# Performance work log

Measured on AMD Instinct MI355X. Metric: run time of the kernel, lower is better.

Reference implementation:

```python
import jax, jax.numpy as jnp
import numpy as np

D_MODEL = 512
NHEAD = 8
HEAD_DIM = D_MODEL // NHEAD
DFF = 2048
RANK = 64
L = 1024
N = 8
EPS = 1e-5


def _layer_norm(x, g, b):
    m = jnp.mean(x, axis=-1, keepdims=True)
    v = jnp.mean(jnp.square(x - m), axis=-1, keepdims=True)
    return (x - m) * jax.lax.rsqrt(v + EPS) * g + b


def setup_inputs() -> dict:
    key = jax.random.key(0)
    ks = jax.random.split(key, 20)
    s = 1.0 / np.sqrt(D_MODEL)
    inp = {
        "q": jax.random.normal(ks[0], (L, N, D_MODEL), jnp.float32),
        "k": jax.random.normal(ks[1], (L, N, D_MODEL), jnp.float32),
        "v": jax.random.normal(ks[2], (L, N, D_MODEL), jnp.float32),
        # attention projections, stored (in, out) so x @ W
        "Wq": jax.random.normal(ks[3], (D_MODEL, D_MODEL), jnp.float32) * s,
        "bq": jnp.zeros((D_MODEL,), jnp.float32),
        "Wk": jax.random.normal(ks[4], (D_MODEL, D_MODEL), jnp.float32) * s,
        "bk": jnp.zeros((D_MODEL,), jnp.float32),
        "Wv": jax.random.normal(ks[5], (D_MODEL, D_MODEL), jnp.float32) * s,
        "bv": jnp.zeros((D_MODEL,), jnp.float32),
        "Wo": jax.random.normal(ks[6], (D_MODEL, D_MODEL), jnp.float32) * s,
        "bo": jnp.zeros((D_MODEL,), jnp.float32),
        "topk": jnp.float32(0.3),  # learned scalar, k = int(S * sigmoid(topk))
        "A1": jax.random.normal(ks[7], (D_MODEL, RANK), jnp.float32) * s,
        "B1": jax.random.normal(ks[8], (RANK, DFF), jnp.float32) / np.sqrt(RANK),
        "A2": jax.random.normal(ks[9], (DFF, RANK), jnp.float32) / np.sqrt(DFF),
        "B2": jax.random.normal(ks[10], (RANK, D_MODEL), jnp.float32) / np.sqrt(RANK),
        "g1": jnp.ones((D_MODEL,), jnp.float32),
        "be1": jnp.zeros((D_MODEL,), jnp.float32),
        "g2": jnp.ones((D_MODEL,), jnp.float32),
        "be2": jnp.zeros((D_MODEL,), jnp.float32),
    }
    return inp


def reference(q, k, v, Wq, bq, Wk, bk, Wv, bv, Wo, bo, topk,
              A1, B1, A2, B2, g1, be1, g2, be2):
    Lq, Nb, E = q.shape
    S = k.shape[0]
    H, Dh = NHEAD, HEAD_DIM

    # projections -> (N, L, H, Dh)
    qh = (q @ Wq + bq).reshape(Lq, Nb, H, Dh).transpose(1, 0, 2, 3)
    kh = (k @ Wk + bk).reshape(S, Nb, H, Dh).transpose(1, 0, 2, 3)
    vh = (v @ Wv + bv).reshape(S, Nb, H, Dh).transpose(1, 0, 2, 3)

    scores = jnp.einsum('nlhd,nshd->nlhs', qh, kh) / jnp.sqrt(jnp.float32(Dh))

    # dynamic top-k mask: keep the k = int(S * sigmoid(topk)) largest per row
    k_keep = (S * jax.nn.sigmoid(topk)).astype(jnp.int32)  # 588 for topk=0.3
    sorted_desc = jnp.sort(scores, axis=-1)[..., ::-1]
    idx = jnp.broadcast_to(k_keep - 1, scores.shape[:-1])[..., None]
    thresh = jnp.take_along_axis(sorted_desc, idx, axis=-1)  # k-th largest
    masked = jnp.where(scores >= thresh, scores, -jnp.inf)
    attn_w = jax.nn.softmax(masked, axis=-1)

    # note original flattens (d, h) order: 'nlhs,nshd->nldh' then view(L,N,E)
    ao = jnp.einsum('nlhs,nshd->nldh', attn_w, vh)
    ao = ao.transpose(1, 0, 2, 3).reshape(Lq, Nb, E)
    attn_out = ao @ Wo + bo

    src = _layer_norm(q + attn_out, g1, be1)
    ffn = jax.nn.relu(src @ A1 @ B1) @ A2 @ B2
    src = _layer_norm(src + ffn, g2, be2)
    return src
```

## Files before the change

### kernel.cpp

```cpp
#include <hip/hip_runtime.h>

typedef unsigned short u16;
typedef unsigned int u32;
typedef unsigned long long u64;
using s16x8 = __attribute__((ext_vector_type(8))) short;
using s16x4 = __attribute__((ext_vector_type(4))) short;
using u16x4 = __attribute__((ext_vector_type(4))) unsigned short;
using u32x4 = __attribute__((ext_vector_type(4))) unsigned int;
using f32x4 = __attribute__((ext_vector_type(4))) float;

__device__ __forceinline__ u16 f2bf(float f) {
  unsigned int u = __float_as_uint(f);
  u += 0x7FFFu + ((u >> 16) & 1u);
  return (u16)(u >> 16);
}
__device__ __forceinline__ float bf2f(u16 b) {
  return __uint_as_float(((u32)b) << 16);
}
__device__ __forceinline__ u32 pkbf(float a, float b) {
  u32 r;
  asm("v_cvt_pk_bf16_f32 %0, %1, %2" : "=v"(r) : "v"(a), "v"(b));
  return r;
}
__device__ __forceinline__ u64 cmp_ge(u32 key, u32 cand) {
  u64 m;
  asm("v_cmp_le_u32 %0, %1, %2" : "=s"(m) : "s"(cand), "v"(key));
  return m;
}
__device__ __forceinline__ u32 f2key(float f) {
  u32 u = __float_as_uint(f);
  u32 flip = (u32)((int)u >> 31) | 0x80000000u;
  return (u ^ flip) >> 16;
}
__device__ __forceinline__ float key2f(u32 k) {
  u32 t = k << 16;
  u32 msk = ((int)t < 0) ? 0x80000000u : 0xFFFF0000u;
  return __uint_as_float(t ^ msk);
}

__global__ __launch_bounds__(256) void prep_w(
    const float* __restrict__ Wq, const float* __restrict__ Wk, const float* __restrict__ Wv,
    const float* __restrict__ Wo, const float* __restrict__ A1, const float* __restrict__ B1,
    const float* __restrict__ A2, const float* __restrict__ B2,
    u16* __restrict__ WqT, u16* __restrict__ WkT, u16* __restrict__ WvT, u16* __restrict__ WoT,
    u16* __restrict__ A1T, u16* __restrict__ B1T, u16* __restrict__ A2T, u16* __restrict__ B2T) {
  __shared__ u16 t[64][68];
  int b = blockIdx.x, tid = threadIdx.x;
  const float* src; u16* dst; int base, R, C;
  if (b < 64)        { src = Wq; dst = WqT; base = 0;   R = 512;  C = 512; }
  else if (b < 128)  { src = Wk; dst = WkT; base = 64;  R = 512;  C = 512; }
  else if (b < 192)  { src = Wv; dst = WvT; base = 128; R = 512;  C = 512; }
  else if (b < 256)  { src = Wo; dst = WoT; base = 192; R = 512;  C = 512; }
  else if (b < 264)  { src = A1; dst = A1T; base = 256; R = 512;  C = 64;  }
  else if (b < 296)  { src = B1; dst = B1T; base = 264; R = 64;   C = 2048;}
  else if (b < 328)  { src = A2; dst = A2T; base = 296; R = 2048; C = 64;  }
  else               { src = B2; dst = B2T; base = 328; R = 64;   C = 512; }
  int ti = b - base;
  int tpr = C >> 6;
  int r0 = (ti / tpr) * 64, c0 = (ti % tpr) * 64;
#pragma unroll
  for (int i = 0; i < 4; ++i) {
    int r = i * 16 + (tid >> 4), c = (tid & 15) * 4;
    float4 f = *(const float4*)&src[(size_t)(r0 + r) * C + c0 + c];
    t[r][c] = f2bf(f.x); t[r][c + 1] = f2bf(f.y);
    t[r][c + 2] = f2bf(f.z); t[r][c + 3] = f2bf(f.w);
  }
  __syncthreads();
#pragma unroll
  for (int i = 0; i < 4; ++i) {
    int cc = i * 16 + (tid >> 4), rr = (tid & 15) * 4;
    u16x4 o;
    o[0] = t[rr][cc]; o[1] = t[rr + 1][cc]; o[2] = t[rr + 2][cc]; o[3] = t[rr + 3][cc];
    *(u16x4*)&dst[(size_t)(c0 + cc) * R + r0 + rr] = o;
  }
}

__global__ __launch_bounds__(256, 4) void qkv_fused(
    const float* __restrict__ q, const float* __restrict__ k, const float* __restrict__ v,
    const u16* __restrict__ WqT, const u16* __restrict__ WkT, const u16* __restrict__ WvT,
    const float* __restrict__ bq, const float* __restrict__ bk, const float* __restrict__ bv,
    u16* __restrict__ Qw, u16* __restrict__ Kw, u16* __restrict__ Vw) {
  __shared__ __align__(16) u16 As[128][72];
  __shared__ __align__(16) u16 Bs[128][72];
  const int z = blockIdx.z;
  const float* A = z == 0 ? q : (z == 1 ? k : v);
  const u16* Bt = z == 0 ? WqT : (z == 1 ? WkT : WvT);
  const float* bias = z == 0 ? bq : (z == 1 ? bk : bv);
  u16* outp = z == 0 ? Qw : (z == 1 ? Kw : Vw);

  const int tid = threadIdx.x;
  const int m0 = blockIdx.y * 128, n0 = blockIdx.x * 128;
  const int lane = tid & 63, wid = tid >> 6;
  const int l16 = lane & 15, hi = lane >> 4;
  const int wr = (wid >> 1) * 64, wc = (wid & 1) * 64;

  f32x4 acc[4][4];
#pragma unroll
  for (int i = 0; i < 4; ++i)
#pragma unroll
    for (int j = 0; j < 4; ++j) acc[i][j] = (f32x4){0.f, 0.f, 0.f, 0.f};

  for (int k0 = 0; k0 < 512; k0 += 64) {
    if (k0) __syncthreads();
#pragma unroll
    for (int i = 0; i < 4; ++i) {
      int idx = i * 256 + tid;
      int r = idx >> 3, cc = (idx & 7) * 8;
      float4 f0 = *(const float4*)&A[(size_t)(m0 + r) * 512 + k0 + cc];
      float4 f1 = *(const float4*)&A[(size_t)(m0 + r) * 512 + k0 + cc + 4];
      u32x4 pk;
      pk[0] = pkbf(f0.x, f0.y); pk[1] = pkbf(f0.z, f0.w);
      pk[2] = pkbf(f1.x, f1.y); pk[3] = pkbf(f1.z, f1.w);
      *(u32x4*)&As[r][cc] = pk;
      *(s16x8*)&Bs[r][cc] = *(const s16x8*)&Bt[(size_t)(n0 + r) * 512 + k0 + cc];
    }
    __syncthreads();
#pragma unroll
    for (int kk = 0; kk < 2; ++kk) {
      const int kb_ = kk * 32 + hi * 8;
      s16x8 af[4], bf[4];
#pragma unroll
      for (int mf = 0; mf < 4; ++mf) af[mf] = *(const s16x8*)&As[wr + mf * 16 + l16][kb_];
#pragma unroll
      for (int nf = 0; nf < 4; ++nf) bf[nf] = *(const s16x8*)&Bs[wc + nf * 16 + l16][kb_];
#pragma unroll
      for (int mf = 0; mf < 4; ++mf)
#pragma unroll
        for (int nf = 0; nf < 4; ++nf)
          acc[mf][nf] = __builtin_amdgcn_mfma_f32_16x16x32_bf16(af[mf], bf[nf], acc[mf][nf], 0, 0, 0);
    }
  }

#pragma unroll
  for (int mf = 0; mf < 4; ++mf)
#pragma unroll
    for (int nf = 0; nf < 4; ++nf)
#pragma unroll
      for (int i = 0; i < 4; ++i) {
        int row = m0 + wr + mf * 16 + hi * 4 + i;
        int col = n0 + wc + nf * 16 + l16;
        float val = acc[mf][nf][i] + bias[col];
        if (z == 0) val *= 0.18033688f;
        int l = row >> 3, n = row & 7, hh = col >> 6, d = col & 63;
        if (z < 2)
          outp[(((size_t)(n * 8 + hh) * 1024 + l) << 6) + d] = f2bf(val);
        else
          outp[((size_t)(n * 8 + hh) * 64 + d) * 1024 + l] = f2bf(val);
      }
}

__global__ __launch_bounds__(512, 8) void attn_kernel(const u16* __restrict__ Qw,
                                                      const u16* __restrict__ Kw,
                                                      const u16* __restrict__ Vw,
                                                      const float* __restrict__ topk,
                                                      u16* __restrict__ ao) {
  __shared__ __align__(16) u16 scb[16 * 1024];
  __shared__ __align__(16) u16 Qt[16][72];
  __shared__ float invs[16];
  const int tid = threadIdx.x, lane = tid & 63, wid = tid >> 6;
  const int l16 = lane & 15, hi = lane >> 4;
  const int mb = blockIdx.x, nh = blockIdx.y;

  const int kkeep = (int)(1024.f / (1.f + __expf(-topk[0])));

  if (tid < 256) {
    int r = tid >> 4, dc = (tid & 15) << 2;
    *(s16x4*)&Qt[r][dc] =
        *(const s16x4*)&Qw[((size_t)nh * 1024 + mb * 16 + r) * 64 + dc];
  }
  __syncthreads();

  {
    const u16* Kb = Kw + (size_t)nh * 1024 * 64;
    s16x8 bq0 = *(const s16x8*)&Qt[l16][hi * 8];
    s16x8 bq1 = *(const s16x8*)&Qt[l16][32 + hi * 8];
    const int s0 = wid * 128;
    const size_t kbase = (size_t)(s0 + l16) * 64 + hi * 8;
    s16x8 c0 = *(const s16x8*)&Kb[kbase];
    s16x8 c1 = *(const s16x8*)&Kb[kbase + 32];
    char* rowq = (char*)scb + l16 * 2048;
    const int Xq = (l16 & 7) << 4;
#pragma unroll
    for (int nf = 0; nf < 8; ++nf) {
      const size_t nb = kbase + (size_t)(nf < 7 ? nf + 1 : nf) * 1024;
      s16x8 n0_ = *(const s16x8*)&Kb[nb];
      s16x8 n1_ = *(const s16x8*)&Kb[nb + 32];
      f32x4 acc = {0.f, 0.f, 0.f, 0.f};
      acc = __builtin_amdgcn_mfma_f32_16x16x32_bf16(c0, bq0, acc, 0, 0, 0);
      acc = __builtin_amdgcn_mfma_f32_16x16x32_bf16(c1, bq1, acc, 0, 0, 0);
      u32 k0 = f2key(acc[0]) | (f2key(acc[1]) << 16);
      u32 k1 = f2key(acc[2]) | (f2key(acc[3]) << 16);
      int boff = (2 * (s0 + nf * 16 + 4 * hi)) ^ Xq;
      *(uint2*)(rowq + boff) = make_uint2(k0, k1);
      c0 = n0_; c1 = n1_;
    }
  }
  __syncthreads();

  for (int rp = 0; rp < 2; ++rp) {
    const int r = wid * 2 + rp;
    char* rb = (char*)scb + r * 2048;
    const int X = (r & 7) << 4;
    const int oa = (16 * lane) ^ X, ob = (16 * lane + 1024) ^ X;
    u32x4 qa = *(const u32x4*)(rb + oa), qb_ = *(const u32x4*)(rb + ob);
    u32 ka[16];
#pragma unroll
    for (int j = 0; j < 4; ++j) {
      ka[2 * j] = qa[j] & 0xFFFFu; ka[2 * j + 1] = qa[j] >> 16;
      ka[8 + 2 * j] = qb_[j] & 0xFFFFu; ka[9 + 2 * j] = qb_[j] >> 16;
    }
    u32 T = 0;
    for (int bit = 15; bit >= 0; --bit) {
      u32 c = T + (1u << bit);
      int n = 0;
#pragma unroll
      for (int j = 0; j < 16; ++j) n += __builtin_popcountll(cmp_ge(ka[j], c));
      T = (n >= kkeep) ? c : T;
    }
    const float tv = key2f(T);
    float s = 0.f;
    u32x4 wa, wb;
#pragma unroll
    for (int j = 0; j < 4; ++j) {
      float e0 = (ka[2 * j] >= T) ? __builtin_amdgcn_exp2f(key2f(ka[2 * j]) - tv) : 0.f;
      float e1 = (ka[2 * j + 1] >= T) ? __builtin_amdgcn_exp2f(key2f(ka[2 * j + 1]) - tv) : 0.f;
      float e2 = (ka[8 + 2 * j] >= T) ? __builtin_amdgcn_exp2f(key2f(ka[8 + 2 * j]) - tv) : 0.f;
      float e3 = (ka[9 + 2 * j] >= T) ? __builtin_amdgcn_exp2f(key2f(ka[9 + 2 * j]) - tv) : 0.f;
      s += e0 + e1 + e2 + e3;
      wa[j] = pkbf(e0, e1); wb[j] = pkbf(e2, e3);
    }
    *(u32x4*)(rb + oa) = wa; *(u32x4*)(rb + ob) = wb;
#pragma unroll
    for (int off = 1; off < 64; off <<= 1) s += __shfl_xor(s, off);
    if (lane == 0) invs[r] = __builtin_amdgcn_rcpf(s);
  }
  __syncthreads();

  if (wid < 4) {
    const u16* Vb = Vw + (size_t)nh * 64 * 1024;
    const int d0 = wid * 16;
    f32x4 oacc0 = {0.f, 0.f, 0.f, 0.f};
    f32x4 oacc1 = {0.f, 0.f, 0.f, 0.f};
    const char* Pbase = (const char*)scb + l16 * 2048;
    const int Xp = (l16 & 7) << 4;
    const size_t vbase = (size_t)(d0 + l16) * 1024 + hi * 8;
    s16x8 v0 = *(const s16x8*)&Vb[vbase];
    s16x8 v1 = *(const s16x8*)&Vb[vbase + 32];
#pragma unroll
    for (int ks = 0; ks < 32; ks += 2) {
      const int kss = ks < 30 ? ks + 2 : ks;
      s16x8 nv0 = *(const s16x8*)&Vb[vbase + (size_t)kss * 32];
      s16x8 nv1 = *(const s16x8*)&Vb[vbase + (size_t)(kss + 1) * 32];
      s16x8 a0 = *(const s16x8*)(Pbase + ((ks * 64 + hi * 16) ^ Xp));
      s16x8 a1 = *(const s16x8*)(Pbase + (((ks + 1) * 64 + hi * 16) ^ Xp));
      oacc0 = __builtin_amdgcn_mfma_f32_16x16x32_bf16(a0, v0, oacc0, 0, 0, 0);
      oacc1 = __builtin_amdgcn_mfma_f32_16x16x32_bf16(a1, v1, oacc1, 0, 0, 0);
      v0 = nv0; v1 = nv1;
    }
    const int n = nh >> 3, hh = nh & 7;
#pragma unroll
    for (int i = 0; i < 4; ++i) {
      int l = mb * 16 + hi * 4 + i;
      int d = d0 + l16;
      float vv = (oacc0[i] + oacc1[i]) * invs[hi * 4 + i];
      ao[(size_t)(l * 8 + n) * 512 + d * 8 + hh] = f2bf(vv);
    }
  }
}

__global__ __launch_bounds__(256, 2) void gemm_ln1(const u16* __restrict__ A,
                                                   const u16* __restrict__ Bt,
                                                   const float* __restrict__ bias,
                                                   const float* __restrict__ residf,
                                                   const float* __restrict__ g,
                                                   const float* __restrict__ be,
                                                   u16* __restrict__ outb) {
  constexpr int K = 512;
  __shared__ __align__(16) u16 As[16][72];
  __shared__ float red_s[4][16];
  __shared__ float red_q[4][16];
  const int tid = threadIdx.x;
  const int lane = tid & 63, wid = tid >> 6;
  const int l16 = lane & 15, hi = lane >> 4;
  const int m0 = blockIdx.x * 16;
  const int wc = wid * 128;

  f32x4 acc[8];
#pragma unroll
  for (int nf = 0; nf < 8; ++nf) acc[nf] = (f32x4){0.f, 0.f, 0.f, 0.f};

  for (int k0 = 0; k0 < K; k0 += 64) {
    if (k0) __syncthreads();
    {
      int r = tid >> 4, c = (tid & 15) << 2;
      *(s16x4*)&As[r][c] = *(const s16x4*)&A[(size_t)(m0 + r) * K + k0 + c];
    }
    __syncthreads();
#pragma unroll
    for (int kk = 0; kk < 2; ++kk) {
      const int kb_ = kk * 32 + hi * 8;
      s16x8 a = *(const s16x8*)&As[l16][kb_];
#pragma unroll
      for (int nf = 0; nf < 8; ++nf) {
        s16x8 b = *(const s16x8*)&Bt[(size_t)(wc + nf * 16 + l16) * K + k0 + kb_];
        acc[nf] = __builtin_amdgcn_mfma_f32_16x16x32_bf16(a, b, acc[nf], 0, 0, 0);
      }
    }
  }

#pragma unroll
  for (int nf = 0; nf < 8; ++nf) {
    int col = wc + nf * 16 + l16;
#pragma unroll
    for (int i = 0; i < 4; ++i) {
      int row = m0 + hi * 4 + i;
      acc[nf][i] += bias[col] + residf[(size_t)row * 512 + col];
    }
  }
  float s[4] = {0.f, 0.f, 0.f, 0.f}, q2[4] = {0.f, 0.f, 0.f, 0.f};
#pragma unroll
  for (int nf = 0; nf < 8; ++nf)
#pragma unroll
    for (int i = 0; i < 4; ++i) {
      s[i] += acc[nf][i];
      q2[i] += acc[nf][i] * acc[nf][i];
    }
#pragma unroll
  for (int i = 0; i < 4; ++i) {
#pragma unroll
    for (int off = 1; off < 16; off <<= 1) {
      s[i] += __shfl_xor(s[i], off);
      q2[i] += __shfl_xor(q2[i], off);
    }
  }
  if (l16 == 0) {
#pragma unroll
    for (int i = 0; i < 4; ++i) {
      red_s[wid][hi * 4 + i] = s[i];
      red_q[wid][hi * 4 + i] = q2[i];
    }
  }
  __syncthreads();
  float mean[4], rstd[4];
#pragma unroll
  for (int i = 0; i < 4; ++i) {
    int r = hi * 4 + i;
    float ms = red_s[0][r] + red_s[1][r] + red_s[2][r] + red_s[3][r];
    float mq = red_q[0][r] + red_q[1][r] + red_q[2][r] + red_q[3][r];
    mean[i] = ms * (1.f / 512.f);
    float var = mq * (1.f / 512.f) - mean[i] * mean[i];
    rstd[i] = rsqrtf(var + 1e-5f);
  }
#pragma unroll
  for (int nf = 0; nf < 8; ++nf) {
    int col = wc + nf * 16 + l16;
    float gv = g[col], bev = be[col];
#pragma unroll
    for (int i = 0; i < 4; ++i) {
      int row = m0 + hi * 4 + i;
      float y = (acc[nf][i] - mean[i]) * rstd[i] * gv + bev;
      outb[(size_t)row * 512 + col] = f2bf(y);
    }
  }
}

__global__ __launch_bounds__(256, 2) void ffn3_ln(const u16* __restrict__ srcb,
                                                  const u16* __restrict__ A1T,
                                                  const u16* __restrict__ B1T,
                                                  const u16* __restrict__ A2T,
                                                  const u16* __restrict__ B2T,
                                                  const float* __restrict__ g,
                                                  const float* __restrict__ be,
                                                  float* __restrict__ outf) {
  __shared__ __align__(16) u16 As[32][72];
  __shared__ __align__(16) u16 Bs[64][72];
  __shared__ __align__(16) u16 Us[32][72];
  __shared__ __align__(16) u16 B1s[64][72];
  __shared__ __align__(16) u16 A2s[64][72];
  __shared__ __align__(16) u16 Hs[32][72];
  __shared__ float red_s[4][32];
  __shared__ float red_q[4][32];
  const int tid = threadIdx.x;
  const int lane = tid & 63, wid = tid >> 6;
  const int l16 = lane & 15, hi = lane >> 4;
  const int m0 = blockIdx.x * 32;
  const int wm = (wid & 1) * 16, wn = (wid >> 1) * 32;

  f32x4 accu[2];
  accu[0] = (f32x4){0.f, 0.f, 0.f, 0.f};
  accu[1] = (f32x4){0.f, 0.f, 0.f, 0.f};
  for (int k0 = 0; k0 < 512; k0 += 64) {
    if (k0) __syncthreads();
    {
      int r = tid >> 3, c = (tid & 7) << 3;
      *(s16x8*)&As[r][c] = *(const s16x8*)&srcb[(size_t)(m0 + r) * 512 + k0 + c];
    }
#pragma unroll
    for (int i = 0; i < 2; ++i) {
      int idx = i * 256 + tid;
      int r = idx >> 3, c = (idx & 7) << 3;
      *(s16x8*)&Bs[r][c] = *(const s16x8*)&A1T[(size_t)r * 512 + k0 + c];
    }
    __syncthreads();
#pragma unroll
    for (int kk = 0; kk < 2; ++kk) {
      const int kb_ = kk * 32 + hi * 8;
      s16x8 a = *(const s16x8*)&As[wm + l16][kb_];
#pragma unroll
      for (int j = 0; j < 2; ++j) {
        s16x8 b = *(const s16x8*)&Bs[wn + j * 16 + l16][kb_];
        accu[j] = __builtin_amdgcn_mfma_f32_16x16x32_bf16(a, b, accu[j], 0, 0, 0);
      }
    }
  }
  __syncthreads();
#pragma unroll
  for (int j = 0; j < 2; ++j)
#pragma unroll
    for (int i = 0; i < 4; ++i)
      Us[wm + hi * 4 + i][wn + j * 16 + l16] = f2bf(accu[j][i]);

  f32x4 w2a[2];
  w2a[0] = (f32x4){0.f, 0.f, 0.f, 0.f};
  w2a[1] = (f32x4){0.f, 0.f, 0.f, 0.f};
  for (int jc = 0; jc < 32; ++jc) {
#pragma unroll
    for (int i = 0; i < 2; ++i) {
      int idx = i * 256 + tid;
      int r = idx >> 3, c = (idx & 7) << 3;
      *(s16x8*)&B1s[r][c] = *(const s16x8*)&B1T[(size_t)(jc * 64 + r) * 64 + c];
      *(s16x8*)&A2s[r][c] = *(const s16x8*)&A2T[(size_t)r * 2048 + jc * 64 + c];
    }
    __syncthreads();
    f32x4 ha[2];
    ha[0] = (f32x4){0.f, 0.f, 0.f, 0.f};
    ha[1] = (f32x4){0.f, 0.f, 0.f, 0.f};
#pragma unroll
    for (int kk = 0; kk < 2; ++kk) {
      const int kb_ = kk * 32 + hi * 8;
      s16x8 a = *(const s16x8*)&Us[wm + l16][kb_];
#pragma unroll
      for (int j = 0; j < 2; ++j) {
        s16x8 b = *(const s16x8*)&B1s[wn + j * 16 + l16][kb_];
        ha[j] = __builtin_amdgcn_mfma_f32_16x16x32_bf16(a, b, ha[j], 0, 0, 0);
      }
    }
#pragma unroll
    for (int j = 0; j < 2; ++j)
#pragma unroll
      for (int i = 0; i < 4; ++i)
        Hs[wm + hi * 4 + i][wn + j * 16 + l16] = f2bf(fmaxf(ha[j][i], 0.f));
    __syncthreads();
#pragma unroll
    for (int kk = 0; kk < 2; ++kk) {
      const int kb_ = kk * 32 + hi * 8;
      s16x8 a = *(const s16x8*)&Hs[wm + l16][kb_];
#pragma unroll
      for (int j = 0; j < 2; ++j) {
        s16x8 b = *(const s16x8*)&A2s[wn + j * 16 + l16][kb_];
        w2a[j] = __builtin_amdgcn_mfma_f32_16x16x32_bf16(a, b, w2a[j], 0, 0, 0);
      }
    }
    __syncthreads();
  }

#pragma unroll
  for (int j = 0; j < 2; ++j)
#pragma unroll
    for (int i = 0; i < 4; ++i)
      As[wm + hi * 4 + i][wn + j * 16 + l16] = f2bf(w2a[j][i]);
  __syncthreads();

  const int wc = wid * 128;
  f32x4 acc[2][8];
#pragma unroll
  for (int mf = 0; mf < 2; ++mf)
#pragma unroll
    for (int nf = 0; nf < 8; ++nf) acc[mf][nf] = (f32x4){0.f, 0.f, 0.f, 0.f};
#pragma unroll
  for (int kk = 0; kk < 2; ++kk) {
    const int kb_ = kk * 32 + hi * 8;
    s16x8 a0 = *(const s16x8*)&As[l16][kb_];
    s16x8 a1 = *(const s16x8*)&As[16 + l16][kb_];
#pragma unroll
    for (int nf = 0; nf < 8; ++nf) {
      s16x8 b = *(const s16x8*)&B2T[(size_t)(wc + nf * 16 + l16) * 64 + kb_];
      acc[0][nf] = __builtin_amdgcn_mfma_f32_16x16x32_bf16(a0, b, acc[0][nf], 0, 0, 0);
      acc[1][nf] = __builtin_amdgcn_mfma_f32_16x16x32_bf16(a1, b, acc[1][nf], 0, 0, 0);
    }
  }
  float s_[2][4], q2_[2][4];
#pragma unroll
  for (int mf = 0; mf < 2; ++mf)
#pragma unroll
    for (int i = 0; i < 4; ++i) { s_[mf][i] = 0.f; q2_[mf][i] = 0.f; }
#pragma unroll
  for (int mf = 0; mf < 2; ++mf)
#pragma unroll
    for (int nf = 0; nf < 8; ++nf) {
      int col = wc + nf * 16 + l16;
#pragma unroll
      for (int i = 0; i < 4; ++i) {
        int row = m0 + mf * 16 + hi * 4 + i;
        float v = acc[mf][nf][i] + bf2f(srcb[(size_t)row * 512 + col]);
        acc[mf][nf][i] = v;
        s_[mf][i] += v;
        q2_[mf][i] += v * v;
      }
    }
#pragma unroll
  for (int mf = 0; mf < 2; ++mf)
#pragma unroll
    for (int i = 0; i < 4; ++i) {
#pragma unroll
      for (int off = 1; off < 16; off <<= 1) {
        s_[mf][i] += __shfl_xor(s_[mf][i], off);
        q2_[mf][i] += __shfl_xor(q2_[mf][i], off);
      }
    }
  if (l16 == 0) {
#pragma unroll
    for (int mf = 0; mf < 2; ++mf)
#pragma unroll
      for (int i = 0; i < 4; ++i) {
        red_s[wid][mf * 16 + hi * 4 + i] = s_[mf][i];
        red_q[wid][mf * 16 + hi * 4 + i] = q2_[mf][i];
      }
  }
  __syncthreads();
  float mean[2][4], rstd[2][4];
#pragma unroll
  for (int mf = 0; mf < 2; ++mf)
#pragma unroll
    for (int i = 0; i < 4; ++i) {
      int r = mf * 16 + hi * 4 + i;
      float ms = red_s[0][r] + red_s[1][r] + red_s[2][r] + red_s[3][r];
      float mq = red_q[0][r] + red_q[1][r] + red_q[2][r] + red_q[3][r];
      mean[mf][i] = ms * (1.f / 512.f);
      float var = mq * (1.f / 512.f) - mean[mf][i] * mean[mf][i];
      rstd[mf][i] = rsqrtf(var + 1e-5f);
    }
#pragma unroll
  for (int mf = 0; mf < 2; ++mf)
#pragma unroll
    for (int nf = 0; nf < 8; ++nf) {
      int col = wc + nf * 16 + l16;
      float gv = g[col], bev = be[col];
#pragma unroll
      for (int i = 0; i < 4; ++i) {
        int row = m0 + mf * 16 + hi * 4 + i;
        float y = (acc[mf][nf][i] - mean[mf][i]) * rstd[mf][i] * gv + bev;
        outf[(size_t)row * 512 + col] = y;
      }
    }
}

extern "C" void kernel_launch(void* const* d_in, const int* in_sizes, int n_in,
                              void* d_out, int out_size, void* d_ws, size_t ws_size,
                              hipStream_t stream) {
  const float* q = (const float*)d_in[0];
  const float* k = (const float*)d_in[1];
  const float* v = (const float*)d_in[2];
  const float* Wq = (const float*)d_in[3];
  const float* bq = (const float*)d_in[4];
  const float* Wk = (const float*)d_in[5];
  const float* bk = (const float*)d_in[6];
  const float* Wv = (const float*)d_in[7];
  const float* bv = (const float*)d_in[8];
  const float* Wo = (const float*)d_in[9];
  const float* bo = (const float*)d_in[10];
  const float* topk = (const float*)d_in[11];
  const float* A1 = (const float*)d_in[12];
  const float* B1 = (const float*)d_in[13];
  const float* A2 = (const float*)d_in[14];
  const float* B2 = (const float*)d_in[15];
  const float* g1 = (const float*)d_in[16];
  const float* be1 = (const float*)d_in[17];
  const float* g2 = (const float*)d_in[18];
  const float* be2 = (const float*)d_in[19];

  char* ws = (char*)d_ws;
  constexpr size_t SZ_TOK_BF = (size_t)8192 * 512 * 2;
  constexpr size_t SZ_W_BF = (size_t)512 * 512 * 2;
  constexpr size_t O_QW = 0;
  constexpr size_t O_KW = O_QW + SZ_TOK_BF;
  constexpr size_t O_VW = O_KW + SZ_TOK_BF;
  constexpr size_t O_WQT = O_VW + SZ_TOK_BF;
  constexpr size_t O_WKT = O_WQT + SZ_W_BF;
  constexpr size_t O_WVT = O_WKT + SZ_W_BF;
  constexpr size_t O_WOT = O_WVT + SZ_W_BF;
  constexpr size_t O_A1T = O_WOT + SZ_W_BF;
  constexpr size_t O_B1T = O_A1T + 65536;
  constexpr size_t O_A2T = O_B1T + 262144;
  constexpr size_t O_B2T = O_A2T + 262144;
  constexpr size_t O_AO = O_B2T + 65536;
  constexpr size_t O_SRCB = O_AO + SZ_TOK_BF;

  u16* Qw_ = (u16*)(ws + O_QW);
  u16* Kw_ = (u16*)(ws + O_KW);
  u16* Vw_ = (u16*)(ws + O_VW);
  u16* WqT = (u16*)(ws + O_WQT);
  u16* WkT = (u16*)(ws + O_WKT);
  u16* WvT = (u16*)(ws + O_WVT);
  u16* WoT = (u16*)(ws + O_WOT);
  u16* A1T = (u16*)(ws + O_A1T);
  u16* B1T = (u16*)(ws + O_B1T);
  u16* A2T = (u16*)(ws + O_A2T);
  u16* B2T = (u16*)(ws + O_B2T);
  u16* ao = (u16*)(ws + O_AO);
  u16* srcb = (u16*)(ws + O_SRCB);

  prep_w<<<336, 256, 0, stream>>>(Wq, Wk, Wv, Wo, A1, B1, A2, B2,
                                  WqT, WkT, WvT, WoT, A1T, B1T, A2T, B2T);

  qkv_fused<<<dim3(4, 64, 3), 256, 0, stream>>>(q, k, v, WqT, WkT, WvT,
                                                bq, bk, bv, Qw_, Kw_, Vw_);

  attn_kernel<<<dim3(64, 64), 512, 0, stream>>>(Qw_, Kw_, Vw_, topk, ao);

  gemm_ln1<<<512, 256, 0, stream>>>(ao, WoT, bo, q, g1, be1, srcb);

  ffn3_ln<<<256, 256, 0, stream>>>(srcb, A1T, B1T, A2T, B2T, g2, be2, (float*)d_out);
}
```

Baseline: 255.3 us.

## Split attention PV over all eight waves and halve FFN row tile

In the attention kernel, the P·V stage now runs on all eight waves instead of four. Each pair of waves splits the key dimension in half, and the partial accumulators are reduced through shared memory with one extra barrier. The fused low-rank FFN+LayerNorm kernel now processes 16 rows per block instead of 32, launching 512 blocks instead of 256, to get more parallelism across CUs. The cost is that each FFN block re-streams the B1/A2 weight tiles for half as many rows, and there is extra LDS and sync overhead in attention.

```diff
diff --git a/kernel.cpp b/kernel.cpp
--- a/kernel.cpp
+++ b/kernel.cpp
@@ -157,6 +157,7 @@
   __shared__ __align__(16) u16 scb[16 * 1024];
   __shared__ __align__(16) u16 Qt[16][72];
   __shared__ float invs[16];
+  __shared__ __align__(16) f32x4 partl[4][64];
   const int tid = threadIdx.x, lane = tid & 63, wid = tid >> 6;
   const int l16 = lane & 15, hi = lane >> 4;
   const int mb = blockIdx.x, nh = blockIdx.y;
@@ -236,19 +237,21 @@
   }
   __syncthreads();
 
-  if (wid < 4) {
+  {
     const u16* Vb = Vw + (size_t)nh * 64 * 1024;
-    const int d0 = wid * 16;
+    const int d0 = (wid & 3) * 16;
+    const int ks0 = (wid >> 2) * 16;
     f32x4 oacc0 = {0.f, 0.f, 0.f, 0.f};
     f32x4 oacc1 = {0.f, 0.f, 0.f, 0.f};
     const char* Pbase = (const char*)scb + l16 * 2048;
     const int Xp = (l16 & 7) << 4;
     const size_t vbase = (size_t)(d0 + l16) * 1024 + hi * 8;
-    s16x8 v0 = *(const s16x8*)&Vb[vbase];
-    s16x8 v1 = *(const s16x8*)&Vb[vbase + 32];
-#pragma unroll
-    for (int ks = 0; ks < 32; ks += 2) {
-      const int kss = ks < 30 ? ks + 2 : ks;
+    s16x8 v0 = *(const s16x8*)&Vb[vbase + (size_t)ks0 * 32];
+    s16x8 v1 = *(const s16x8*)&Vb[vbase + (size_t)(ks0 + 1) * 32];
+#pragma unroll
+    for (int kt = 0; kt < 16; kt += 2) {
+      const int ks = ks0 + kt;
+      const int kss = (kt < 14) ? ks + 2 : ks;
       s16x8 nv0 = *(const s16x8*)&Vb[vbase + (size_t)kss * 32];
       s16x8 nv1 = *(const s16x8*)&Vb[vbase + (size_t)(kss + 1) * 32];
       s16x8 a0 = *(const s16x8*)(Pbase + ((ks * 64 + hi * 16) ^ Xp));
@@ -257,13 +260,21 @@
       oacc1 = __builtin_amdgcn_mfma_f32_16x16x32_bf16(a1, v1, oacc1, 0, 0, 0);
       v0 = nv0; v1 = nv1;
     }
-    const int n = nh >> 3, hh = nh & 7;
-#pragma unroll
-    for (int i = 0; i < 4; ++i) {
-      int l = mb * 16 + hi * 4 + i;
-      int d = d0 + l16;
-      float vv = (oacc0[i] + oacc1[i]) * invs[hi * 4 + i];
-      ao[(size_t)(l * 8 + n) * 512 + d * 8 + hh] = f2bf(vv);
+    f32x4 part;
+#pragma unroll
+    for (int i = 0; i < 4; ++i) part[i] = oacc0[i] + oacc1[i];
+    if (wid >= 4) partl[wid - 4][lane] = part;
+    __syncthreads();
+    if (wid < 4) {
+      f32x4 other = partl[wid][lane];
+      const int n = nh >> 3, hh = nh & 7;
+#pragma unroll
+      for (int i = 0; i < 4; ++i) {
+        int l = mb * 16 + hi * 4 + i;
+        int d = d0 + l16;
+        float vv = (part[i] + other[i]) * invs[hi * 4 + i];
+        ao[(size_t)(l * 8 + n) * 512 + d * 8 + hh] = f2bf(vv);
+      }
     }
   }
 }
@@ -372,28 +383,26 @@
                                                   const float* __restrict__ g,
                                                   const float* __restrict__ be,
                                                   float* __restrict__ outf) {
-  __shared__ __align__(16) u16 As[32][72];
+  __shared__ __align__(16) u16 As[16][72];
   __shared__ __align__(16) u16 Bs[64][72];
-  __shared__ __align__(16) u16 Us[32][72];
+  __shared__ __align__(16) u16 Us[16][72];
   __shared__ __align__(16) u16 B1s[64][72];
   __shared__ __align__(16) u16 A2s[64][72];
-  __shared__ __align__(16) u16 Hs[32][72];
-  __shared__ float red_s[4][32];
-  __shared__ float red_q[4][32];
+  __shared__ __align__(16) u16 Hs[16][72];
+  __shared__ float red_s[4][16];
+  __shared__ float red_q[4][16];
   const int tid = threadIdx.x;
   const int lane = tid & 63, wid = tid >> 6;
   const int l16 = lane & 15, hi = lane >> 4;
-  const int m0 = blockIdx.x * 32;
-  const int wm = (wid & 1) * 16, wn = (wid >> 1) * 32;
-
-  f32x4 accu[2];
-  accu[0] = (f32x4){0.f, 0.f, 0.f, 0.f};
-  accu[1] = (f32x4){0.f, 0.f, 0.f, 0.f};
+  const int m0 = blockIdx.x * 16;
+  const int wn = wid * 16;
+
+  f32x4 accu = (f32x4){0.f, 0.f, 0.f, 0.f};
   for (int k0 = 0; k0 < 512; k0 += 64) {
     if (k0) __syncthreads();
     {
-      int r = tid >> 3, c = (tid & 7) << 3;
-      *(s16x8*)&As[r][c] = *(const s16x8*)&srcb[(size_t)(m0 + r) * 512 + k0 + c];
+      int r = tid >> 4, c = (tid & 15) << 2;
+      *(s16x4*)&As[r][c] = *(const s16x4*)&srcb[(size_t)(m0 + r) * 512 + k0 + c];
     }
 #pragma unroll
     for (int i = 0; i < 2; ++i) {
@@ -405,24 +414,17 @@
 #pragma unroll
     for (int kk = 0; kk < 2; ++kk) {
       const int kb_ = kk * 32 + hi * 8;
-      s16x8 a = *(const s16x8*)&As[wm + l16][kb_];
-#pragma unroll
-      for (int j = 0; j < 2; ++j) {
-        s16x8 b = *(const s16x8*)&Bs[wn + j * 16 + l16][kb_];
-        accu[j] = __builtin_amdgcn_mfma_f32_16x16x32_bf16(a, b, accu[j], 0, 0, 0);
-      }
-    }
-  }
-  __syncthreads();
-#pragma unroll
-  for (int j = 0; j < 2; ++j)
-#pragma unroll
-    for (int i = 0; i < 4; ++i)
-      Us[wm + hi * 4 + i][wn + j * 16 + l16] = f2bf(accu[j][i]);
-
-  f32x4 w2a[2];
-  w2a[0] = (f32x4){0.f, 0.f, 0.f, 0.f};
-  w2a[1] = (f32x4){0.f, 0.f, 0.f, 0.f};
+      s16x8 a = *(const s16x8*)&As[l16][kb_];
+      s16x8 b = *(const s16x8*)&Bs[wn + l16][kb_];
+      accu = __builtin_amdgcn_mfma_f32_16x16x32_bf16(a, b, accu, 0, 0, 0);
+    }
+  }
+  __syncthreads();
+#pragma unroll
+  for (int i = 0; i < 4; ++i)
+    Us[hi * 4 + i][wn + l16] = f2bf(accu[i]);
+
+  f32x4 w2a = (f32x4){0.f, 0.f, 0.f, 0.f};
   for (int jc = 0; jc < 32; ++jc) {
 #pragma unroll
     for (int i = 0; i < 2; ++i) {
@@ -432,127 +434,97 @@
       *(s16x8*)&A2s[r][c] = *(const s16x8*)&A2T[(size_t)r * 2048 + jc * 64 + c];
     }
     __syncthreads();
-    f32x4 ha[2];
-    ha[0] = (f32x4){0.f, 0.f, 0.f, 0.f};
-    ha[1] = (f32x4){0.f, 0.f, 0.f, 0.f};
+    f32x4 ha = (f32x4){0.f, 0.f, 0.f, 0.f};
 #pragma unroll
     for (int kk = 0; kk < 2; ++kk) {
       const int kb_ = kk * 32 + hi * 8;
-      s16x8 a = *(const s16x8*)&Us[wm + l16][kb_];
-#pragma unroll
-      for (int j = 0; j < 2; ++j) {
-        s16x8 b = *(const s16x8*)&B1s[wn + j * 16 + l16][kb_];
-        ha[j] = __builtin_amdgcn_mfma_f32_16x16x32_bf16(a, b, ha[j], 0, 0, 0);
-      }
-    }
-#pragma unroll
-    for (int j = 0; j < 2; ++j)
-#pragma unroll
-      for (int i = 0; i < 4; ++i)
-        Hs[wm + hi * 4 + i][wn + j * 16 + l16] = f2bf(fmaxf(ha[j][i], 0.f));
+      s16x8 a = *(const s16x8*)&Us[l16][kb_];
+      s16x8 b = *(const s16x8*)&B1s[wn + l16][kb_];
+      ha = __builtin_amdgcn_mfma_f32_16x16x32_bf16(a, b, ha, 0, 0, 0);
+    }
+#pragma unroll
+    for (int i = 0; i < 4; ++i)
+      Hs[hi * 4 + i][wn + l16] = f2bf(fmaxf(ha[i], 0.f));
     __syncthreads();
 #pragma unroll
     for (int kk = 0; kk < 2; ++kk) {
       const int kb_ = kk * 32 + hi * 8;
-      s16x8 a = *(const s16x8*)&Hs[wm + l16][kb_];
-#pragma unroll
-      for (int j = 0; j < 2; ++j) {
-        s16x8 b = *(const s16x8*)&A2s[wn + j * 16 + l16][kb_];
-        w2a[j] = __builtin_amdgcn_mfma_f32_16x16x32_bf16(a, b, w2a[j], 0, 0, 0);
-      }
-    }
-    __syncthreads();
-  }
-
-#pragma unroll
-  for (int j = 0; j < 2; ++j)
-#pragma unroll
-    for (int i = 0; i < 4; ++i)
-      As[wm + hi * 4 + i][wn + j * 16 + l16] = f2bf(w2a[j][i]);
+      s16x8 a = *(const s16x8*)&Hs[l16][kb_];
+      s16x8 b = *(const s16x8*)&A2s[wn + l16][kb_];
+      w2a = __builtin_amdgcn_mfma_f32_16x16x32_bf16(a, b, w2a, 0, 0, 0);
+    }
+    __syncthreads();
+  }
+
+#pragma unroll
+  for (int i = 0; i < 4; ++i)
+    As[hi * 4 + i][wn + l16] = f2bf(w2a[i]);
   __syncthreads();
 
   const int wc = wid * 128;
-  f32x4 acc[2][8];
-#pragma unroll
-  for (int mf = 0; mf < 2; ++mf)
-#pragma unroll
-    for (int nf = 0; nf < 8; ++nf) acc[mf][nf] = (f32x4){0.f, 0.f, 0.f, 0.f};
+  f32x4 acc[8];
+#pragma unroll
+  for (int nf = 0; nf < 8; ++nf) acc[nf] = (f32x4){0.f, 0.f, 0.f, 0.f};
 #pragma unroll
   for (int kk = 0; kk < 2; ++kk) {
     const int kb_ = kk * 32 + hi * 8;
-    s16x8 a0 = *(const s16x8*)&As[l16][kb_];
-    s16x8 a1 = *(const s16x8*)&As[16 + l16][kb_];
+    s16x8 a = *(const s16x8*)&As[l16][kb_];
 #pragma unroll
     for (int nf = 0; nf < 8; ++nf) {
       s16x8 b = *(const s16x8*)&B2T[(size_t)(wc + nf * 16 + l16) * 64 + kb_];
-      acc[0][nf] = __builtin_amdgcn_mfma_f32_16x16x32_bf16(a0, b, acc[0][nf], 0, 0, 0);
-      acc[1][nf] = __builtin_amdgcn_mfma_f32_16x16x32_bf16(a1, b, acc[1][nf], 0, 0, 0);
-    }
-  }
-  float s_[2][4], q2_[2][4];
-#pragma unroll
-  for (int mf = 0; mf < 2; ++mf)
-#pragma unroll
-    for (int i = 0; i < 4; ++i) { s_[mf][i] = 0.f; q2_[mf][i] = 0.f; }
-#pragma unroll
-  for (int mf = 0; mf < 2; ++mf)
-#pragma unroll
-    for (int nf = 0; nf < 8; ++nf) {
-      int col = wc + nf * 16 + l16;
-#pragma unroll
-      for (int i = 0; i < 4; ++i) {
-        int row = m0 + mf * 16 + hi * 4 + i;
-        float v = acc[mf][nf][i] + bf2f(srcb[(size_t)row * 512 + col]);
-        acc[mf][nf][i] = v;
-        s_[mf][i] += v;
-        q2_[mf][i] += v * v;
-      }
-    }
-#pragma unroll
-  for (int mf = 0; mf < 2; ++mf)
-#pragma unroll
-    for (int i = 0; i < 4; ++i) {
-#pragma unroll
-      for (int off = 1; off < 16; off <<= 1) {
-        s_[mf][i] += __shfl_xor(s_[mf][i], off);
-        q2_[mf][i] += __shfl_xor(q2_[mf][i], off);
-      }
-    }
+      acc[nf] = __builtin_amdgcn_mfma_f32_16x16x32_bf16(a, b, acc[nf], 0, 0, 0);
+    }
+  }
+  float s_[4] = {0.f, 0.f, 0.f, 0.f}, q2_[4] = {0.f, 0.f, 0.f, 0.f};
+#pragma unroll
+  for (int nf = 0; nf < 8; ++nf) {
+    int col = wc + nf * 16 + l16;
+#pragma unroll
+    for (int i = 0; i < 4; ++i) {
+      int row = m0 + hi * 4 + i;
+      float v = acc[nf][i] + bf2f(srcb[(size_t)row * 512 + col]);
+      acc[nf][i] = v;
+      s_[i] += v;
+      q2_[i] += v * v;
+    }
+  }
+#pragma unroll
+  for (int i = 0; i < 4; ++i) {
+#pragma unroll
+    for (int off = 1; off < 16; off <<= 1) {
+      s_[i] += __shfl_xor(s_[i], off);
+      q2_[i] += __shfl_xor(q2_[i], off);
+    }
+  }
   if (l16 == 0) {
 #pragma unroll
-    for (int mf = 0; mf < 2; ++mf)
-#pragma unroll
-      for (int i = 0; i < 4; ++i) {
-        red_s[wid][mf * 16 + hi * 4 + i] = s_[mf][i];
-        red_q[wid][mf * 16 + hi * 4 + i] = q2_[mf][i];
-      }
-  }
-  __syncthreads();
-  float mean[2][4], rstd[2][4];
-#pragma unroll
-  for (int mf = 0; mf < 2; ++mf)
-#pragma unroll
-    for (int i = 0; i < 4; ++i) {
-      int r = mf * 16 + hi * 4 + i;
-      float ms = red_s[0][r] + red_s[1][r] + red_s[2][r] + red_s[3][r];
-      float mq = red_q[0][r] + red_q[1][r] + red_q[2][r] + red_q[3][r];
-      mean[mf][i] = ms * (1.f / 512.f);
-      float var = mq * (1.f / 512.f) - mean[mf][i] * mean[mf][i];
-      rstd[mf][i] = rsqrtf(var + 1e-5f);
-    }
-#pragma unroll
-  for (int mf = 0; mf < 2; ++mf)
-#pragma unroll
-    for (int nf = 0; nf < 8; ++nf) {
-      int col = wc + nf * 16 + l16;
-      float gv = g[col], bev = be[col];
-#pragma unroll
-      for (int i = 0; i < 4; ++i) {
-        int row = m0 + mf * 16 + hi * 4 + i;
-        float y = (acc[mf][nf][i] - mean[mf][i]) * rstd[mf][i] * gv + bev;
-        outf[(size_t)row * 512 + col] = y;
-      }
-    }
+    for (int i = 0; i < 4; ++i) {
+      red_s[wid][hi * 4 + i] = s_[i];
+      red_q[wid][hi * 4 + i] = q2_[i];
+    }
+  }
+  __syncthreads();
+  float mean[4], rstd[4];
+#pragma unroll
+  for (int i = 0; i < 4; ++i) {
+    int r = hi * 4 + i;
+    float ms = red_s[0][r] + red_s[1][r] + red_s[2][r] + red_s[3][r];
+    float mq = red_q[0][r] + red_q[1][r] + red_q[2][r] + red_q[3][r];
+    mean[i] = ms * (1.f / 512.f);
+    float var = mq * (1.f / 512.f) - mean[i] * mean[i];
+    rstd[i] = rsqrtf(var + 1e-5f);
+  }
+#pragma unroll
+  for (int nf = 0; nf < 8; ++nf) {
+    int col = wc + nf * 16 + l16;
+    float gv = g[col], bev = be[col];
+#pragma unroll
+    for (int i = 0; i < 4; ++i) {
+      int row = m0 + hi * 4 + i;
+      float y = (acc[nf][i] - mean[i]) * rstd[i] * gv + bev;
+      outf[(size_t)row * 512 + col] = y;
+    }
+  }
 }
 
 extern "C" void kernel_launch(void* const* d_in, const int* in_sizes, int n_in,
@@ -620,5 +592,5 @@
 
   gemm_ln1<<<512, 256, 0, stream>>>(ao, WoT, bo, q, g1, be1, srcb);
 
-  ffn3_ln<<<256, 256, 0, stream>>>(srcb, A1T, B1T, A2T, B2T, g2, be2, (float*)d_out);
-}
+  ffn3_ln<<<512, 256, 0, stream>>>(srcb, A1T, B1T, A2T, B2T, g2, be2, (float*)d_out);
+}
```

After: 250.8 us, median of 2. No clear change (-1.8%).
